# Optimization experiments

Hardware: AMD Instinct MI355X
Metric: run time of the kernel (lower is better)

## Reference

```python
import jax, jax.numpy as jnp
import numpy as np

EPS = 1e-8
LEAK = 0.2


def upsample_linear_2x(x):
    # PyTorch nn.Upsample(scale_factor=2, mode='linear', align_corners=False) on [B,C,L]
    B, C, L = x.shape
    Lo = 2 * L
    coords = jnp.maximum((jnp.arange(Lo, dtype=jnp.float32) + 0.5) / 2.0 - 0.5, 0.0)
    i0 = jnp.minimum(jnp.floor(coords).astype(jnp.int32), L - 1)
    i1 = jnp.minimum(i0 + 1, L - 1)
    w = (coords - i0.astype(jnp.float32)).astype(x.dtype)
    return x[..., i0] * (1.0 - w) + x[..., i1] * w


def mod_conv1d(x, style, W, demod=True):
    # Style-modulated conv (StyleGAN2 Conv2DMod adapted to 1D).
    # x: [B,C,L], style: [B,C], W: [F,C,K]. Equivalent to per-sample weight
    # W*(style+1) (optionally demodulated) via input scaling + shared conv.
    s = style + 1.0
    pad = (W.shape[-1] - 1) // 2
    y = jax.lax.conv_general_dilated(x * s[:, :, None], W, (1,), [(pad, pad)],
                                     dimension_numbers=('NCH', 'OIH', 'NCH'))
    if demod:
        wmod = W[None] * s[:, None, :, None]              # [B,F,C,K]
        d = jax.lax.rsqrt(jnp.sum(wmod * wmod, axis=(2, 3)) + EPS)  # [B,F]
        y = y * d[:, :, None]
    return y


def setup_inputs() -> dict:
    key = jax.random.key(0)
    ks = jax.random.split(key, 12)
    B, Cin, F, L, Z = 8, 256, 128, 2048, 256
    Lu = 2 * L
    inp = {}
    inp['x'] = jax.random.normal(ks[0], (B, Cin, L), jnp.float32)
    inp['prev_rgb'] = jax.random.normal(ks[1], (B, 1, Lu), jnp.float32)
    inp['istyle'] = jax.random.normal(ks[2], (B, Z), jnp.float32)
    inp['inoise'] = jax.random.normal(ks[3], (B, 100), jnp.float32)
    # learned parameters
    inp['style1_w'] = jax.random.normal(ks[4], (Cin, Z), jnp.float32) * 0.02
    inp['style1_b'] = jnp.zeros((Cin,), jnp.float32)
    inp['conv1_w'] = jax.random.normal(ks[5], (F, Cin, 3), jnp.float32) * 0.05
    inp['noise_w1'] = jax.random.normal(ks[6], (F * Lu, 100), jnp.float32) * 0.01
    inp['style2_w'] = jax.random.normal(ks[7], (F, Z), jnp.float32) * 0.02
    inp['style2_b'] = jnp.zeros((F,), jnp.float32)
    inp['conv2_w'] = jax.random.normal(ks[8], (F, F, 3), jnp.float32) * 0.05
    inp['noise_w2'] = jax.random.normal(ks[9], (F * Lu, 100), jnp.float32) * 0.01
    inp['rgb_style_w'] = jax.random.normal(ks[10], (F, Z), jnp.float32) * 0.02
    inp['rgb_style_b'] = jnp.zeros((F,), jnp.float32)
    inp['rgb_conv_w'] = jax.random.normal(ks[11], (1, F, 1), jnp.float32) * 0.05
    return inp


def reference(x, prev_rgb, istyle, inoise, style1_w, style1_b, conv1_w, noise_w1,
              style2_w, style2_b, conv2_w, noise_w2, rgb_style_w, rgb_style_b, rgb_conv_w):
    x = upsample_linear_2x(x)                                 # [B,Cin,Lu]
    s1 = istyle @ style1_w.T + style1_b                       # [B,Cin]
    x = mod_conv1d(x, s1, conv1_w, demod=True)                # [B,F,Lu]
    n1 = (inoise @ noise_w1.T).reshape(x.shape)               # noise injection 1
    x = jax.nn.leaky_relu(x + n1, LEAK)
    s2 = istyle @ style2_w.T + style2_b                       # [B,F]
    x = mod_conv1d(x, s2, conv2_w, demod=True)                # [B,F,Lu]
    n2 = (inoise @ noise_w2.T).reshape(x.shape)               # noise injection 2
    x = jax.nn.leaky_relu(x + n2, LEAK)
    srgb = istyle @ rgb_style_w.T + rgb_style_b               # [B,F]
    rgb = jnp.einsum('bcl,fc->bfl', x * (srgb + 1.0)[:, :, None], rgb_conv_w[:, :, 0])
    rgb = rgb + prev_rgb
    rgb = upsample_linear_2x(rgb)                             # [B,1,2*Lu]
    return (x, rgb)
```

## Files before the change

kernel.cpp:

```cpp
#include <hip/hip_runtime.h>
#include <hip/hip_bf16.h>

#define EPS 1e-8f
#define LEAK 0.2f

#define B 8
#define CIN 256
#define F 128
#define L 2048
#define LU 4096
#define Z 256
#define NZ 100
#define S (F * LU)

typedef __attribute__((ext_vector_type(8))) short bf16x8;
typedef __attribute__((ext_vector_type(4))) float f32x4;

__device__ inline unsigned short f2bf(float x) {
    unsigned u = __builtin_bit_cast(unsigned, x);
    u += 0x7fffu + ((u >> 16) & 1u);
    return (unsigned short)(u >> 16);
}
__device__ inline float bf2f(unsigned short h) {
    unsigned u = ((unsigned)h) << 16;
    return __builtin_bit_cast(float, u);
}
__device__ inline void gload_lds16(const void* g, void* l) {
    __builtin_amdgcn_global_load_lds((const __attribute__((address_space(1))) void*)g,
                                     (__attribute__((address_space(3))) void*)l, 16, 0, 0);
}

__global__ void k_styles(const float* __restrict__ istyle,
                         const float* __restrict__ s1w, const float* __restrict__ s1b,
                         const float* __restrict__ s2w, const float* __restrict__ s2b,
                         const float* __restrict__ rgbw, const float* __restrict__ rgbb,
                         const float* __restrict__ rgbcw,
                         const float* __restrict__ W1, const float* __restrict__ W2,
                         float* __restrict__ s1, float* __restrict__ s2,
                         float* __restrict__ srgbS,
                         float* __restrict__ d1, float* __restrict__ d2,
                         unsigned short* __restrict__ Wt1, unsigned short* __restrict__ Wt2) {
    int t = threadIdx.x;
    {
        int i = blockIdx.x * 256 + t;
        if (i < 3 * F * CIN) {
            int kk = i / (F * CIN);
            int rem = i - kk * (F * CIN);
            int f = rem >> 8, c = rem & 255;
            Wt1[i] = f2bf(W1[(f * CIN + c) * 3 + kk]);
        }
        if (i < 3 * F * F) {
            int kk = i / (F * F);
            int rem = i - kk * (F * F);
            int f = rem >> 7, c = rem & 127;
            Wt2[i] = f2bf(W2[(f * F + c) * 3 + kk]);
        }
    }
    if (blockIdx.x >= 8) return;
    __shared__ float is[Z];
    __shared__ float sh1[CIN];
    __shared__ float sh2[F];
    int b = blockIdx.x;
    if (t < Z) is[t] = istyle[b * Z + t];
    __syncthreads();
    {
        float acc = 0.f;
        const float* w = s1w + (size_t)t * Z;
        for (int z = 0; z < Z; z += 4) {
            float4 v = *(const float4*)(w + z);
            acc += v.x * is[z] + v.y * is[z + 1] + v.z * is[z + 2] + v.w * is[z + 3];
        }
        float v = acc + s1b[t] + 1.0f;
        sh1[t] = v;
        s1[b * CIN + t] = v;
    }
    if (t < F) {
        float a2 = 0.f, a3 = 0.f;
        const float* w2 = s2w + (size_t)t * Z;
        const float* w3 = rgbw + (size_t)t * Z;
        for (int z = 0; z < Z; z += 4) {
            float4 u2 = *(const float4*)(w2 + z);
            float4 u3 = *(const float4*)(w3 + z);
            a2 += u2.x * is[z] + u2.y * is[z + 1] + u2.z * is[z + 2] + u2.w * is[z + 3];
            a3 += u3.x * is[z] + u3.y * is[z + 1] + u3.z * is[z + 2] + u3.w * is[z + 3];
        }
        float v2 = a2 + s2b[t] + 1.0f;
        sh2[t] = v2;
        s2[b * F + t] = v2;
        srgbS[b * F + t] = (a3 + rgbb[t] + 1.0f) * rgbcw[t];
    }
    __syncthreads();
    if (t < F) {
        float acc = 0.f;
        const float* w = W1 + (size_t)t * CIN * 3;
        for (int c = 0; c < CIN; c += 4) {
            float4 va = *(const float4*)(w + c * 3);
            float4 vb = *(const float4*)(w + c * 3 + 4);
            float4 vc = *(const float4*)(w + c * 3 + 8);
            float s0 = sh1[c], s1v = sh1[c + 1], s2v = sh1[c + 2], s3 = sh1[c + 3];
            acc += s0 * s0 * (va.x * va.x + va.y * va.y + va.z * va.z);
            acc += s1v * s1v * (va.w * va.w + vb.x * vb.x + vb.y * vb.y);
            acc += s2v * s2v * (vb.z * vb.z + vb.w * vb.w + vc.x * vc.x);
            acc += s3 * s3 * (vc.y * vc.y + vc.z * vc.z + vc.w * vc.w);
        }
        d1[b * F + t] = rsqrtf(acc + EPS);
    } else {
        int f = t - F;
        float acc = 0.f;
        const float* w = W2 + (size_t)f * F * 3;
        for (int c = 0; c < F; c += 4) {
            float4 va = *(const float4*)(w + c * 3);
            float4 vb = *(const float4*)(w + c * 3 + 4);
            float4 vc = *(const float4*)(w + c * 3 + 8);
            float s0 = sh2[c], s1v = sh2[c + 1], s2v = sh2[c + 2], s3 = sh2[c + 3];
            acc += s0 * s0 * (va.x * va.x + va.y * va.y + va.z * va.z);
            acc += s1v * s1v * (va.w * va.w + vb.x * vb.x + vb.y * vb.y);
            acc += s2v * s2v * (vb.z * vb.z + vb.w * vb.w + vc.x * vc.x);
            acc += s3 * s3 * (vc.y * vc.y + vc.z * vc.z + vc.w * vc.w);
        }
        d2[b * F + f] = rsqrtf(acc + EPS);
    }
}

__global__ __launch_bounds__(256) void k_prepx(const float* __restrict__ x,
                                               const float* __restrict__ s1,
                                               unsigned short* __restrict__ xt) {
    int b = blockIdx.z, c0 = blockIdx.y * 64, l0 = blockIdx.x * 64;
    int t = threadIdx.x;
    __shared__ float xj[64][37];
    int j0 = (l0 >> 1) - 1;
    for (int idx = t; idx < 64 * 34; idx += 256) {
        int c = idx / 34, jj = idx - c * 34;
        int j = j0 + jj;
        j = j < 0 ? 0 : (j > L - 1 ? L - 1 : j);
        xj[c][jj] = x[((size_t)(b * CIN + c0 + c)) * L + j];
    }
    __syncthreads();
    int c = t & 63;
    int lg = t >> 6;
    float s = s1[b * CIN + c0 + c];
    for (int li = 0; li < 16; ++li) {
        int ll = lg * 16 + li;
        int l = l0 + ll;
        int j = l >> 1;
        int jj = j - j0;
        float v;
        if (l & 1) {
            v = 0.75f * xj[c][jj] + 0.25f * xj[c][jj + 1];
        } else {
            v = (j == 0) ? xj[c][jj] : (0.25f * xj[c][jj - 1] + 0.75f * xj[c][jj]);
        }
        xt[((size_t)(b * LU + l)) * CIN + c0 + c] = f2bf(v * s);
    }
}

__global__ __launch_bounds__(256) void k_conv1(const unsigned short* __restrict__ xt,
                                               const unsigned short* __restrict__ Wt1,
                                               const float* __restrict__ d1,
                                               unsigned short* __restrict__ y1) {
    const int b0 = blockIdx.y * 2;
    const int l0 = blockIdx.x * 64;
    const int nfb = blockIdx.z * 4;
    const int lane = threadIdx.x & 63, wv = threadIdx.x >> 6;
    const int lbase = l0 + wv * 16;
    const int m = lane & 15, ks = lane >> 4;

    f32x4 acc[2][4];
#pragma unroll
    for (int bb = 0; bb < 2; ++bb)
#pragma unroll
        for (int nf = 0; nf < 4; ++nf) acc[bb][nf] = (f32x4)0.f;

    const unsigned short* xb0 = xt + ((size_t)(b0 + 0) * LU) * CIN + ks * 8;
    const unsigned short* xb1 = xt + ((size_t)(b0 + 1) * LU) * CIN + ks * 8;

#pragma unroll 2
    for (int kc = 0; kc < 8; ++kc) {
#pragma unroll
        for (int kk = 0; kk < 3; ++kk) {
            int lA = lbase + m + kk - 1;
            bf16x8 a0 = (bf16x8)0, a1 = (bf16x8)0;
            if (lA >= 0 && lA < LU) {
                a0 = *(const bf16x8*)&xb0[(size_t)lA * CIN + kc * 32];
                a1 = *(const bf16x8*)&xb1[(size_t)lA * CIN + kc * 32];
            }
#pragma unroll
            for (int nf = 0; nf < 4; ++nf) {
                const bf16x8 w =
                    *(const bf16x8*)&Wt1[((kk * F + (nfb + nf) * 16 + m) << 8) + kc * 32 + ks * 8];
                acc[0][nf] = __builtin_amdgcn_mfma_f32_16x16x32_bf16(a0, w, acc[0][nf], 0, 0, 0);
                acc[1][nf] = __builtin_amdgcn_mfma_f32_16x16x32_bf16(a1, w, acc[1][nf], 0, 0, 0);
            }
        }
    }
#pragma unroll
    for (int bb = 0; bb < 2; ++bb) {
        int b = b0 + bb;
#pragma unroll
        for (int nf = 0; nf < 4; ++nf) {
            int f = (nfb + nf) * 16 + m;
            float dm = d1[b * F + f];
#pragma unroll
            for (int q = 0; q < 4; ++q) {
                int l = lbase + ks * 4 + q;
                y1[((size_t)(b * LU + l) << 7) + f] = f2bf(acc[bb][nf][q] * dm);
            }
        }
    }
}

__global__ __launch_bounds__(256) void k_noise1(unsigned short* y1,
                                                const float* __restrict__ nw,
                                                const float* __restrict__ inoise,
                                                const float* __restrict__ s2) {
    __shared__ float lds[2][6400];
    const int t = threadIdx.x;
    const int rr = t & 63;
    const int b0 = (t >> 6) * 2;
    const bool w0 = (t >> 6) == 0;
    const float* inb = inoise + __builtin_amdgcn_readfirstlane(b0) * NZ;
    const int f0 = (blockIdx.x >> 8) * 32;
    const int l0 = (blockIdx.x & 255) * 16;
    const int fseg = rr >> 1, dl = rr & 1;
    const int f = f0 + fseg;

    const float s2v0 = s2[b0 * F + f];
    const float s2v1 = s2[(b0 + 1) * F + f];
    unsigned short yv0[8], yv1[8];
#pragma unroll
    for (int cc = 0; cc < 8; ++cc) {
        int l = l0 + 2 * cc + dl;
        size_t i = (size_t)l * F + f;
        yv0[cc] = y1[(size_t)b0 * S + i];
        yv1[cc] = y1[(size_t)(b0 + 1) * S + i];
    }

    auto stage = [&](int buf, int cc) {
        const int lbase = l0 + 2 * cc;
#pragma unroll
        for (int r = 0; r < 7; ++r) {
            int g = r * 256 + t;
            if (g < 1600) {
                int fs = g / 50;
                int rem = g - fs * 50;
                int d2 = (rem >= 25) ? 1 : 0;
                int m = rem - 25 * d2;
                const float* src = nw + ((size_t)(f0 + fs) * LU + lbase + d2) * NZ + m * 4;
                gload_lds16(src, &lds[buf][g * 4]);
            }
        }
    };

    auto compute = [&](int buf, int cc) {
        const float* rp = &lds[buf][rr * 100];
        float a0 = 0.f, a1 = 0.f;
#pragma unroll
        for (int q = 0; q < 25; ++q) {
            float4 v = *(const float4*)&rp[q * 4];
            int z = q * 4;
            a0 += v.x * inb[z] + v.y * inb[z + 1] + v.z * inb[z + 2] + v.w * inb[z + 3];
            a1 += v.x * inb[NZ + z] + v.y * inb[NZ + z + 1] + v.z * inb[NZ + z + 2] +
                  v.w * inb[NZ + z + 3];
        }
        const int l = l0 + 2 * cc + dl;
        const size_t i = (size_t)l * F + f;
        float val0 = bf2f(yv0[cc]) + a0;
        val0 = val0 >= 0.f ? val0 : LEAK * val0;
        y1[(size_t)b0 * S + i] = f2bf(val0 * s2v0);
        float val1 = bf2f(yv1[cc]) + a1;
        val1 = val1 >= 0.f ? val1 : LEAK * val1;
        y1[(size_t)(b0 + 1) * S + i] = f2bf(val1 * s2v1);
    };

    stage(0, 0);
    stage(1, 1);

#define WSTEP(N0, N1)                                                       \
    if (w0) { asm volatile("s_waitcnt vmcnt(" #N0 ")" ::: "memory"); }      \
    else    { asm volatile("s_waitcnt vmcnt(" #N1 ")" ::: "memory"); }      \
    __builtin_amdgcn_s_barrier();                                           \
    __builtin_amdgcn_sched_barrier(0);

    WSTEP(7, 6)              compute(0, 0);
    WSTEP(2, 2) stage(0, 2); compute(1, 1);
    WSTEP(2, 2) stage(1, 3); compute(0, 2);
    WSTEP(2, 2) stage(0, 4); compute(1, 3);
    WSTEP(2, 2) stage(1, 5); compute(0, 4);
    WSTEP(2, 2) stage(0, 6); compute(1, 5);
    WSTEP(2, 2) stage(1, 7); compute(0, 6);
    WSTEP(2, 2)              compute(1, 7);
#undef WSTEP
}

__global__ __launch_bounds__(256) void k_conv2(const unsigned short* __restrict__ y1n,
                                               const unsigned short* __restrict__ Wt2,
                                               const float* __restrict__ d2,
                                               float* __restrict__ xout) {
    const int b0 = blockIdx.y * 2;
    const int l0 = blockIdx.x * 64;
    const int mfb = blockIdx.z * 4;
    const int lane = threadIdx.x & 63, wv = threadIdx.x >> 6;
    const int lbase = l0 + wv * 16;
    const int m = lane & 15, ks = lane >> 4;

    f32x4 acc[2][4];
#pragma unroll
    for (int bb = 0; bb < 2; ++bb)
#pragma unroll
        for (int mf = 0; mf < 4; ++mf) acc[bb][mf] = (f32x4)0.f;

    const unsigned short* yb0 = y1n + ((size_t)(b0 + 0) * LU) * F + ks * 8;
    const unsigned short* yb1 = y1n + ((size_t)(b0 + 1) * LU) * F + ks * 8;

#pragma unroll 2
    for (int kc = 0; kc < 4; ++kc) {
#pragma unroll
        for (int kk = 0; kk < 3; ++kk) {
            int lB = lbase + m + kk - 1;
            bf16x8 bv0 = (bf16x8)0, bv1 = (bf16x8)0;
            if (lB >= 0 && lB < LU) {
                bv0 = *(const bf16x8*)&yb0[(size_t)lB * F + kc * 32];
                bv1 = *(const bf16x8*)&yb1[(size_t)lB * F + kc * 32];
            }
#pragma unroll
            for (int mf = 0; mf < 4; ++mf) {
                const bf16x8 w =
                    *(const bf16x8*)&Wt2[((kk * F + (mfb + mf) * 16 + m) << 7) + kc * 32 + ks * 8];
                acc[0][mf] = __builtin_amdgcn_mfma_f32_16x16x32_bf16(w, bv0, acc[0][mf], 0, 0, 0);
                acc[1][mf] = __builtin_amdgcn_mfma_f32_16x16x32_bf16(w, bv1, acc[1][mf], 0, 0, 0);
            }
        }
    }
#pragma unroll
    for (int bb = 0; bb < 2; ++bb) {
        int b = b0 + bb;
#pragma unroll
        for (int mf = 0; mf < 4; ++mf) {
#pragma unroll
            for (int q = 0; q < 4; ++q) {
                int f = (mfb + mf) * 16 + ks * 4 + q;
                int l = lbase + m;
                xout[((size_t)(b * F + f) << 12) + l] = acc[bb][mf][q] * d2[b * F + f];
            }
        }
    }
}

__global__ __launch_bounds__(256) void k_noise2(const float* __restrict__ nw,
                                                const float* __restrict__ inoise,
                                                float* xio) {
    __shared__ float lds[2][6400];
    const int t = threadIdx.x;
    const int rr = t & 63;
    const int b0 = (t >> 6) * 2;
    const bool w0 = (t >> 6) == 0;
    const float* inb = inoise + __builtin_amdgcn_readfirstlane(b0) * NZ;
    const int row0 = blockIdx.x * 512;

    float xv0[8], xv1[8];
#pragma unroll
    for (int cc = 0; cc < 8; ++cc) {
        size_t i = (size_t)row0 + cc * 64 + rr;
        xv0[cc] = xio[(size_t)b0 * S + i];
        xv1[cc] = xio[(size_t)(b0 + 1) * S + i];
    }

    auto stage = [&](int buf, int cc) {
        const float* src0 = nw + ((size_t)row0 + cc * 64) * NZ;
#pragma unroll
        for (int r = 0; r < 7; ++r) {
            int g = r * 256 + t;
            if (g < 1600) gload_lds16(src0 + g * 4, &lds[buf][g * 4]);
        }
    };

    auto compute = [&](int buf, int cc) {
        const float* rp = &lds[buf][rr * 100];
        float a0 = 0.f, a1 = 0.f;
#pragma unroll
        for (int q = 0; q < 25; ++q) {
            float4 v = *(const float4*)&rp[q * 4];
            int z = q * 4;
            a0 += v.x * inb[z] + v.y * inb[z + 1] + v.z * inb[z + 2] + v.w * inb[z + 3];
            a1 += v.x * inb[NZ + z] + v.y * inb[NZ + z + 1] + v.z * inb[NZ + z + 2] +
                  v.w * inb[NZ + z + 3];
        }
        const size_t i = (size_t)row0 + cc * 64 + rr;
        float val0 = xv0[cc] + a0;
        val0 = val0 >= 0.f ? val0 : LEAK * val0;
        xio[(size_t)b0 * S + i] = val0;
        float val1 = xv1[cc] + a1;
        val1 = val1 >= 0.f ? val1 : LEAK * val1;
        xio[(size_t)(b0 + 1) * S + i] = val1;
    };

    stage(0, 0);
    stage(1, 1);

#define WSTEP(N0, N1)                                                       \
    if (w0) { asm volatile("s_waitcnt vmcnt(" #N0 ")" ::: "memory"); }      \
    else    { asm volatile("s_waitcnt vmcnt(" #N1 ")" ::: "memory"); }      \
    __builtin_amdgcn_s_barrier();                                           \
    __builtin_amdgcn_sched_barrier(0);

    WSTEP(7, 6)              compute(0, 0);
    WSTEP(2, 2) stage(0, 2); compute(1, 1);
    WSTEP(2, 2) stage(1, 3); compute(0, 2);
    WSTEP(2, 2) stage(0, 4); compute(1, 3);
    WSTEP(2, 2) stage(1, 5); compute(0, 4);
    WSTEP(2, 2) stage(0, 6); compute(1, 5);
    WSTEP(2, 2) stage(1, 7); compute(0, 6);
    WSTEP(2, 2)              compute(1, 7);
#undef WSTEP
}

__global__ __launch_bounds__(256) void k_rgb(const float* __restrict__ xf,
                                             const float* __restrict__ srgbS,
                                             const float* __restrict__ prev,
                                             float* __restrict__ rgb) {
    int b = blockIdx.y;
    int o0 = blockIdx.x * 512;
    int t = threadIdx.x;
    __shared__ float ss[F];
    __shared__ float pre[258];
    if (t < F) ss[t] = srgbS[b * F + t];
    __syncthreads();
    int j0 = (o0 >> 1) - 1;
    for (int jj = t; jj < 258; jj += 256) {
        int j = j0 + jj;
        j = j < 0 ? 0 : (j > LU - 1 ? LU - 1 : j);
        float acc = prev[b * LU + j];
        const float* xb = xf + (size_t)b * S + j;
        for (int f = 0; f < F; ++f) acc += xb[(size_t)f * LU] * ss[f];
        pre[jj] = acc;
    }
    __syncthreads();
    int jj = t + 1;
    int j = j0 + jj;
    float ve = (j == 0) ? pre[jj] : (0.25f * pre[jj - 1] + 0.75f * pre[jj]);
    float vo = 0.75f * pre[jj] + 0.25f * pre[jj + 1];
    float2 v2 = make_float2(ve, vo);
    *(float2*)&rgb[(size_t)b * 2 * LU + o0 + 2 * t] = v2;
}

extern "C" void kernel_launch(void* const* d_in, const int* in_sizes, int n_in,
                              void* d_out, int out_size, void* d_ws, size_t ws_size,
                              hipStream_t stream) {
    const float* x      = (const float*)d_in[0];
    const float* prev   = (const float*)d_in[1];
    const float* istyle = (const float*)d_in[2];
    const float* inoise = (const float*)d_in[3];
    const float* s1w    = (const float*)d_in[4];
    const float* s1b    = (const float*)d_in[5];
    const float* W1     = (const float*)d_in[6];
    const float* nw1    = (const float*)d_in[7];
    const float* s2w    = (const float*)d_in[8];
    const float* s2b    = (const float*)d_in[9];
    const float* W2     = (const float*)d_in[10];
    const float* nw2    = (const float*)d_in[11];
    const float* rgbw   = (const float*)d_in[12];
    const float* rgbb   = (const float*)d_in[13];
    const float* rgbcw  = (const float*)d_in[14];

    char* w = (char*)d_ws;
    float* s1      = (float*)(w);
    float* s2      = (float*)(w + 8 * 1024);
    float* srgbS   = (float*)(w + 12 * 1024);
    float* d1      = (float*)(w + 16 * 1024);
    float* d2      = (float*)(w + 20 * 1024);
    unsigned short* Wt1 = (unsigned short*)(w + 256 * 1024);
    unsigned short* Wt2 = (unsigned short*)(w + 448 * 1024);
    unsigned short* y1  = (unsigned short*)(w + (size_t)1024 * 1024);

    unsigned short* xt = (unsigned short*)d_out;

    float* xout   = (float*)d_out;
    float* rgbout = xout + (size_t)B * S;

    k_styles<<<384, 256, 0, stream>>>(istyle, s1w, s1b, s2w, s2b, rgbw, rgbb, rgbcw,
                                      W1, W2, s1, s2, srgbS, d1, d2, Wt1, Wt2);
    k_prepx<<<dim3(LU / 64, CIN / 64, B), 256, 0, stream>>>(x, s1, xt);
    k_conv1<<<dim3(LU / 64, B / 2, 2), 256, 0, stream>>>(xt, Wt1, d1, y1);
    k_noise1<<<1024, 256, 0, stream>>>(y1, nw1, inoise, s2);
    k_conv2<<<dim3(LU / 64, B / 2, 2), 256, 0, stream>>>(y1, Wt2, d2, xout);
    k_noise2<<<1024, 256, 0, stream>>>(nw2, inoise, xout);
    k_rgb<<<dim3(2 * LU / 512, B), 256, 0, stream>>>(xout, srgbS, prev, rgbout);
}
```

Baseline: 239.5 us.

## Compute noise-injection matvecs with bf16 MFMA instead of scalar FMA loops

Both noise kernels now compute the inoise @ noise_w product for all 8 batches with 16x16x32 bf16 MFMA instructions. The noise weight rows staged in LDS are converted to bf16 fragments on the fly, and the inoise rows are preloaded as A fragments padded to 16 rows. Before, each wave handled two batches with scalar FMAs. The aim is to cut the ALU work, which may be the bottleneck after the weight stream. The cost is bf16 rounding of the noise weights and inputs, half-empty MFMA tiles from the padding, and retuned vmcnt waits.

```diff
diff --git a/kernel.cpp b/kernel.cpp
--- a/kernel.cpp
+++ b/kernel.cpp
@@ -24,6 +24,18 @@
 __device__ inline float bf2f(unsigned short h) {
     unsigned u = ((unsigned)h) << 16;
     return __builtin_bit_cast(float, u);
+}
+__device__ inline unsigned pack2(float a, float b) {
+    __hip_bfloat162 h = __float22bfloat162_rn(make_float2(a, b));
+    unsigned u;
+    __builtin_memcpy(&u, &h, 4);
+    return u;
+}
+__device__ inline bf16x8 cvtfrag(float4 a, float4 b) {
+    uint4 u;
+    u.x = pack2(a.x, a.y); u.y = pack2(a.z, a.w);
+    u.z = pack2(b.x, b.y); u.w = pack2(b.z, b.w);
+    return __builtin_bit_cast(bf16x8, u);
 }
 __device__ inline void gload_lds16(const void* g, void* l) {
     __builtin_amdgcn_global_load_lds((const __attribute__((address_space(1))) void*)g,
@@ -215,31 +227,49 @@
                                                 const float* __restrict__ s2) {
     __shared__ float lds[2][6400];
     const int t = threadIdx.x;
-    const int rr = t & 63;
-    const int b0 = (t >> 6) * 2;
+    const int lane = t & 63, wv = t >> 6;
+    const int n = lane & 15, ks = lane >> 4;
     const bool w0 = (t >> 6) == 0;
-    const float* inb = inoise + __builtin_amdgcn_readfirstlane(b0) * NZ;
     const int f0 = (blockIdx.x >> 8) * 32;
     const int l0 = (blockIdx.x & 255) * 16;
-    const int fseg = rr >> 1, dl = rr & 1;
+    const int r = wv * 16 + n;
+    const int fseg = r >> 1, dl = r & 1;
     const int f = f0 + fseg;
 
-    const float s2v0 = s2[b0 * F + f];
-    const float s2v1 = s2[(b0 + 1) * F + f];
-    unsigned short yv0[8], yv1[8];
-#pragma unroll
-    for (int cc = 0; cc < 8; ++cc) {
-        int l = l0 + 2 * cc + dl;
-        size_t i = (size_t)l * F + f;
-        yv0[cc] = y1[(size_t)b0 * S + i];
-        yv1[cc] = y1[(size_t)(b0 + 1) * S + i];
+    bf16x8 af[4];
+#pragma unroll
+    for (int ck = 0; ck < 4; ++ck) {
+        bf16x8 a = (bf16x8)0;
+        if (n < 8) {
+            const float* ap = inoise + n * NZ;
+#pragma unroll
+            for (int j = 0; j < 8; ++j) {
+                int z = ck * 32 + ks * 8 + j;
+                if (z < NZ) a[j] = (short)f2bf(ap[z]);
+            }
+        }
+        af[ck] = a;
+    }
+
+    unsigned short yv[8][4] = {};
+    float s2v[4] = {};
+    if (ks < 2) {
+#pragma unroll
+        for (int q = 0; q < 4; ++q) s2v[q] = s2[(ks * 4 + q) * F + f];
+#pragma unroll
+        for (int cc = 0; cc < 8; ++cc) {
+            int l = l0 + 2 * cc + dl;
+            size_t i = (size_t)l * F + f;
+#pragma unroll
+            for (int q = 0; q < 4; ++q) yv[cc][q] = y1[(size_t)(ks * 4 + q) * S + i];
+        }
     }
 
     auto stage = [&](int buf, int cc) {
         const int lbase = l0 + 2 * cc;
 #pragma unroll
-        for (int r = 0; r < 7; ++r) {
-            int g = r * 256 + t;
+        for (int rr = 0; rr < 7; ++rr) {
+            int g = rr * 256 + t;
             if (g < 1600) {
                 int fs = g / 50;
                 int rem = g - fs * 50;
@@ -252,24 +282,34 @@
     };
 
     auto compute = [&](int buf, int cc) {
-        const float* rp = &lds[buf][rr * 100];
-        float a0 = 0.f, a1 = 0.f;
-#pragma unroll
-        for (int q = 0; q < 25; ++q) {
-            float4 v = *(const float4*)&rp[q * 4];
-            int z = q * 4;
-            a0 += v.x * inb[z] + v.y * inb[z + 1] + v.z * inb[z + 2] + v.w * inb[z + 3];
-            a1 += v.x * inb[NZ + z] + v.y * inb[NZ + z + 1] + v.z * inb[NZ + z + 2] +
-                  v.w * inb[NZ + z + 3];
-        }
-        const int l = l0 + 2 * cc + dl;
-        const size_t i = (size_t)l * F + f;
-        float val0 = bf2f(yv0[cc]) + a0;
-        val0 = val0 >= 0.f ? val0 : LEAK * val0;
-        y1[(size_t)b0 * S + i] = f2bf(val0 * s2v0);
-        float val1 = bf2f(yv1[cc]) + a1;
-        val1 = val1 >= 0.f ? val1 : LEAK * val1;
-        y1[(size_t)(b0 + 1) * S + i] = f2bf(val1 * s2v1);
+        const float* rowp = &lds[buf][r * 100];
+        f32x4 acc = (f32x4)0.f;
+#pragma unroll
+        for (int ck = 0; ck < 3; ++ck) {
+            float4 u0 = *(const float4*)&rowp[ck * 32 + ks * 8];
+            float4 u1 = *(const float4*)&rowp[ck * 32 + ks * 8 + 4];
+            acc = __builtin_amdgcn_mfma_f32_16x16x32_bf16(af[ck], cvtfrag(u0, u1), acc, 0, 0, 0);
+        }
+        {
+            bf16x8 b3 = (bf16x8)0;
+            if (ks == 0) {
+                float4 u = *(const float4*)&rowp[96];
+                unsigned p0 = pack2(u.x, u.y), p1 = pack2(u.z, u.w);
+                b3[0] = (short)(p0 & 0xffff); b3[1] = (short)(p0 >> 16);
+                b3[2] = (short)(p1 & 0xffff); b3[3] = (short)(p1 >> 16);
+            }
+            acc = __builtin_amdgcn_mfma_f32_16x16x32_bf16(af[3], b3, acc, 0, 0, 0);
+        }
+        if (ks < 2) {
+            const int l = l0 + 2 * cc + dl;
+            const size_t i = (size_t)l * F + f;
+#pragma unroll
+            for (int q = 0; q < 4; ++q) {
+                float val = bf2f(yv[cc][q]) + acc[q];
+                val = val >= 0.f ? val : LEAK * val;
+                y1[(size_t)(ks * 4 + q) * S + i] = f2bf(val * s2v[q]);
+            }
+        }
     };
 
     stage(0, 0);
@@ -282,13 +322,13 @@
     __builtin_amdgcn_sched_barrier(0);
 
     WSTEP(7, 6)              compute(0, 0);
-    WSTEP(2, 2) stage(0, 2); compute(1, 1);
-    WSTEP(2, 2) stage(1, 3); compute(0, 2);
-    WSTEP(2, 2) stage(0, 4); compute(1, 3);
-    WSTEP(2, 2) stage(1, 5); compute(0, 4);
-    WSTEP(2, 2) stage(0, 6); compute(1, 5);
-    WSTEP(2, 2) stage(1, 7); compute(0, 6);
-    WSTEP(2, 2)              compute(1, 7);
+    WSTEP(4, 4) stage(0, 2); compute(1, 1);
+    WSTEP(4, 4) stage(1, 3); compute(0, 2);
+    WSTEP(4, 4) stage(0, 4); compute(1, 3);
+    WSTEP(4, 4) stage(1, 5); compute(0, 4);
+    WSTEP(4, 4) stage(0, 6); compute(1, 5);
+    WSTEP(4, 4) stage(1, 7); compute(0, 6);
+    WSTEP(4, 4)              compute(1, 7);
 #undef WSTEP
 }
 
@@ -351,47 +391,74 @@
                                                 float* xio) {
     __shared__ float lds[2][6400];
     const int t = threadIdx.x;
-    const int rr = t & 63;
-    const int b0 = (t >> 6) * 2;
+    const int lane = t & 63, wv = t >> 6;
+    const int n = lane & 15, ks = lane >> 4;
     const bool w0 = (t >> 6) == 0;
-    const float* inb = inoise + __builtin_amdgcn_readfirstlane(b0) * NZ;
     const int row0 = blockIdx.x * 512;
-
-    float xv0[8], xv1[8];
-#pragma unroll
-    for (int cc = 0; cc < 8; ++cc) {
-        size_t i = (size_t)row0 + cc * 64 + rr;
-        xv0[cc] = xio[(size_t)b0 * S + i];
-        xv1[cc] = xio[(size_t)(b0 + 1) * S + i];
+    const int r = wv * 16 + n;
+
+    bf16x8 af[4];
+#pragma unroll
+    for (int ck = 0; ck < 4; ++ck) {
+        bf16x8 a = (bf16x8)0;
+        if (n < 8) {
+            const float* ap = inoise + n * NZ;
+#pragma unroll
+            for (int j = 0; j < 8; ++j) {
+                int z = ck * 32 + ks * 8 + j;
+                if (z < NZ) a[j] = (short)f2bf(ap[z]);
+            }
+        }
+        af[ck] = a;
+    }
+
+    float xv[8][4] = {};
+    if (ks < 2) {
+#pragma unroll
+        for (int cc = 0; cc < 8; ++cc) {
+            size_t i = (size_t)row0 + cc * 64 + r;
+#pragma unroll
+            for (int q = 0; q < 4; ++q) xv[cc][q] = xio[(size_t)(ks * 4 + q) * S + i];
+        }
     }
 
     auto stage = [&](int buf, int cc) {
         const float* src0 = nw + ((size_t)row0 + cc * 64) * NZ;
 #pragma unroll
-        for (int r = 0; r < 7; ++r) {
-            int g = r * 256 + t;
+        for (int rr = 0; rr < 7; ++rr) {
+            int g = rr * 256 + t;
             if (g < 1600) gload_lds16(src0 + g * 4, &lds[buf][g * 4]);
         }
     };
 
     auto compute = [&](int buf, int cc) {
-        const float* rp = &lds[buf][rr * 100];
-        float a0 = 0.f, a1 = 0.f;
-#pragma unroll
-        for (int q = 0; q < 25; ++q) {
-            float4 v = *(const float4*)&rp[q * 4];
-            int z = q * 4;
-            a0 += v.x * inb[z] + v.y * inb[z + 1] + v.z * inb[z + 2] + v.w * inb[z + 3];
-            a1 += v.x * inb[NZ + z] + v.y * inb[NZ + z + 1] + v.z * inb[NZ + z + 2] +
-                  v.w * inb[NZ + z + 3];
-        }
-        const size_t i = (size_t)row0 + cc * 64 + rr;
-        float val0 = xv0[cc] + a0;
-        val0 = val0 >= 0.f ? val0 : LEAK * val0;
-        xio[(size_t)b0 * S + i] = val0;
-        float val1 = xv1[cc] + a1;
-        val1 = val1 >= 0.f ? val1 : LEAK * val1;
-        xio[(size_t)(b0 + 1) * S + i] = val1;
+        const float* rowp = &lds[buf][r * 100];
+        f32x4 acc = (f32x4)0.f;
+#pragma unroll
+        for (int ck = 0; ck < 3; ++ck) {
+            float4 u0 = *(const float4*)&rowp[ck * 32 + ks * 8];
+            float4 u1 = *(const float4*)&rowp[ck * 32 + ks * 8 + 4];
+            acc = __builtin_amdgcn_mfma_f32_16x16x32_bf16(af[ck], cvtfrag(u0, u1), acc, 0, 0, 0);
+        }
+        {
+            bf16x8 b3 = (bf16x8)0;
+            if (ks == 0) {
+                float4 u = *(const float4*)&rowp[96];
+                unsigned p0 = pack2(u.x, u.y), p1 = pack2(u.z, u.w);
+                b3[0] = (short)(p0 & 0xffff); b3[1] = (short)(p0 >> 16);
+                b3[2] = (short)(p1 & 0xffff); b3[3] = (short)(p1 >> 16);
+            }
+            acc = __builtin_amdgcn_mfma_f32_16x16x32_bf16(af[3], b3, acc, 0, 0, 0);
+        }
+        if (ks < 2) {
+            const size_t i = (size_t)row0 + cc * 64 + r;
+#pragma unroll
+            for (int q = 0; q < 4; ++q) {
+                float val = xv[cc][q] + acc[q];
+                val = val >= 0.f ? val : LEAK * val;
+                xio[(size_t)(ks * 4 + q) * S + i] = val;
+            }
+        }
     };
 
     stage(0, 0);
@@ -404,13 +471,13 @@
     __builtin_amdgcn_sched_barrier(0);
 
     WSTEP(7, 6)              compute(0, 0);
-    WSTEP(2, 2) stage(0, 2); compute(1, 1);
-    WSTEP(2, 2) stage(1, 3); compute(0, 2);
-    WSTEP(2, 2) stage(0, 4); compute(1, 3);
-    WSTEP(2, 2) stage(1, 5); compute(0, 4);
-    WSTEP(2, 2) stage(0, 6); compute(1, 5);
-    WSTEP(2, 2) stage(1, 7); compute(0, 6);
-    WSTEP(2, 2)              compute(1, 7);
+    WSTEP(4, 4) stage(0, 2); compute(1, 1);
+    WSTEP(4, 4) stage(1, 3); compute(0, 2);
+    WSTEP(4, 4) stage(0, 4); compute(1, 3);
+    WSTEP(4, 4) stage(1, 5); compute(0, 4);
+    WSTEP(4, 4) stage(0, 6); compute(1, 5);
+    WSTEP(4, 4) stage(1, 7); compute(0, 6);
+    WSTEP(4, 4)              compute(1, 7);
 #undef WSTEP
 }
 
```

Result: no change. 239.5 us (+0.0%).
